# Kernel optimization log

Hardware: AMD Instinct MI355X
Metric: run time of the kernel (lower is better)

Reference implementation:

```python
import jax, jax.numpy as jnp
import numpy as np

N_NODES = 1_000_000
N_EDGES = 20_000_000


def setup_inputs() -> dict:
    key = jax.random.key(0)
    k_row, k_col, k_attr = jax.random.split(key, 3)
    # Guarantee every row appears at least once so row-sums are > 0
    # (the original module implicitly assumes no zero-degree rows).
    row_tail = jax.random.randint(k_row, (N_EDGES - N_NODES,), 0, N_NODES, dtype=jnp.int32)
    row = jnp.concatenate([jnp.arange(N_NODES, dtype=jnp.int32), row_tail])
    col = jax.random.randint(k_col, (N_EDGES,), 0, N_NODES, dtype=jnp.int32)
    edge_index = jnp.stack([row, col])  # [2, E]
    # Positive edge weights keep the reciprocal well-conditioned.
    edge_attr = jax.random.uniform(k_attr, (N_EDGES,), dtype=jnp.float32,
                                   minval=0.1, maxval=1.0)
    return {"edge_index": edge_index, "edge_attr": edge_attr, "N": N_NODES}


def reference(edge_index, edge_attr, N):
    # spmm(edge_index, edge_attr, N, N, ones) == per-row sum of edge weights
    rowsum = jax.ops.segment_sum(edge_attr, edge_index[0], num_segments=N)  # [N]
    rownorm = 1.0 / rowsum                                                  # [N]
    # Gather normalization factor at the COLUMN index of each edge, then scale.
    return rownorm[edge_index[1]] * edge_attr                                # [E]
```

## Files before the change

### kernel.cpp

```cpp
#include <hip/hip_runtime.h>
#include <stdint.h>


typedef int      v4i __attribute__((ext_vector_type(4)));
typedef float    v4f __attribute__((ext_vector_type(4)));
typedef unsigned v4u __attribute__((ext_vector_type(4)));
using ull = unsigned long long;

#define BKT_BITS 13
#define BKT_W    (1 << BKT_BITS)
#define NB       128
#define NMAX     (NB << BKT_BITS)
#define TILE     4096
#define BLOCK1   512
#define BLOCK2   1024


__global__ __launch_bounds__(BLOCK1) void hist_kernel(
    const int* __restrict__ row, int* __restrict__ histG, int E)
{
    __shared__ int h[NB];
    const int t = threadIdx.x;
    const long base = (long)blockIdx.x * TILE;
    if (t < NB) h[t] = 0;
    __syncthreads();
    if (base + TILE <= (long)E) {
        #pragma unroll
        for (int k = 0; k < 2; ++k) {
            const long e0 = base + ((long)(k * BLOCK1 + t) << 2);
            const v4i rv = *reinterpret_cast<const v4i*>(row + e0);
            atomicAdd(&h[rv.x >> BKT_BITS], 1);
            atomicAdd(&h[rv.y >> BKT_BITS], 1);
            atomicAdd(&h[rv.z >> BKT_BITS], 1);
            atomicAdd(&h[rv.w >> BKT_BITS], 1);
        }
    } else {
        for (int k = 0; k < 2; ++k) {
            const long e0 = base + ((long)(k * BLOCK1 + t) << 2);
            for (int j = 0; j < 4; ++j)
                if (e0 + j < (long)E) atomicAdd(&h[row[e0 + j] >> BKT_BITS], 1);
        }
    }
    __syncthreads();
    if (t < NB) histG[(size_t)blockIdx.x * NB + t] = h[t];
}

__global__ __launch_bounds__(256) void totals_kernel(
    const int* __restrict__ histG, int* __restrict__ totals, int nTiles)
{
    __shared__ int s[256];
    const int b = blockIdx.x;
    int acc = 0;
    for (int t = threadIdx.x; t < nTiles; t += 256)
        acc += histG[(size_t)t * NB + b];
    s[threadIdx.x] = acc;
    __syncthreads();
    for (int o = 128; o > 0; o >>= 1) {
        if (threadIdx.x < o) s[threadIdx.x] += s[threadIdx.x + o];
        __syncthreads();
    }
    if (threadIdx.x == 0) totals[b] = s[0];
}

__global__ __launch_bounds__(NB) void bases_kernel(
    const int* __restrict__ totals, int* __restrict__ bases)
{
    __shared__ int s[NB];
    const int t = threadIdx.x;
    const int rc = (totals[t] + 1) & ~1;
    s[t] = rc;
    __syncthreads();
    for (int off = 1; off < NB; off <<= 1) {
        const int v = (t >= off) ? s[t - off] : 0;
        __syncthreads();
        s[t] += v;
        __syncthreads();
    }
    bases[t] = s[t] - rc;
}

__global__ __launch_bounds__(256) void offsets_kernel(
    const int* __restrict__ histG, const int* __restrict__ bases,
    int* __restrict__ offG, int nTiles)
{
    __shared__ int s[256];
    const int b = blockIdx.x;
    const int seg = (nTiles + 255) >> 8;
    const int t0 = threadIdx.x * seg;
    int acc = 0;
    for (int k = 0; k < seg; ++k) {
        const int t = t0 + k;
        if (t < nTiles) acc += histG[(size_t)t * NB + b];
    }
    s[threadIdx.x] = acc;
    __syncthreads();
    for (int off = 1; off < 256; off <<= 1) {
        const int v = (threadIdx.x >= off) ? s[threadIdx.x - off] : 0;
        __syncthreads();
        s[threadIdx.x] += v;
        __syncthreads();
    }
    int run = bases[b] + s[threadIdx.x] - acc;
    for (int k = 0; k < seg; ++k) {
        const int t = t0 + k;
        if (t < nTiles) {
            offG[(size_t)t * NB + b] = run;
            run += histG[(size_t)t * NB + b];
        }
    }
}

__global__ __launch_bounds__(BLOCK1) void scatter_kernel(
    const int* __restrict__ row, const float* __restrict__ attr,
    const int* __restrict__ offG, ull* __restrict__ pairsG, int E)
{
    __shared__ int cnt[NB];
    __shared__ int scanb[NB];
    __shared__ int gbase[NB];
    __shared__ ull pairs[TILE];

    const int  t    = threadIdx.x;
    const long base = (long)blockIdx.x * TILE;
    const bool full = (base + TILE <= (long)E);

    if (t < NB) cnt[t] = 0;
    __syncthreads();

    int r[8]; float a[8]; int rk[8];
    if (full) {
        #pragma unroll
        for (int k = 0; k < 2; ++k) {
            const long e0 = base + ((long)(k * BLOCK1 + t) << 2);
            const v4i rv = *reinterpret_cast<const v4i*>(row + e0);
            const v4f av = __builtin_nontemporal_load(reinterpret_cast<const v4f*>(attr + e0));
            r[k*4+0]=rv.x; r[k*4+1]=rv.y; r[k*4+2]=rv.z; r[k*4+3]=rv.w;
            a[k*4+0]=av.x; a[k*4+1]=av.y; a[k*4+2]=av.z; a[k*4+3]=av.w;
        }
        #pragma unroll
        for (int i = 0; i < 8; ++i)
            rk[i] = atomicAdd(&cnt[r[i] >> BKT_BITS], 1);
    } else {
        for (int k = 0; k < 2; ++k) {
            const long e0 = base + ((long)(k * BLOCK1 + t) << 2);
            for (int j = 0; j < 4; ++j) {
                const int i = k*4 + j;
                if (e0 + j < (long)E) {
                    r[i] = row[e0 + j]; a[i] = attr[e0 + j];
                    rk[i] = atomicAdd(&cnt[r[i] >> BKT_BITS], 1);
                } else r[i] = -1;
            }
        }
    }
    __syncthreads();

    if (t < 64) {
        const int h0 = cnt[2*t], h1 = cnt[2*t+1];
        const int sum = h0 + h1;
        int x = sum;
        #pragma unroll
        for (int off = 1; off < 64; off <<= 1) {
            const int y = __shfl_up(x, off);
            if (t >= off) x += y;
        }
        const int excl = x - sum;
        scanb[2*t]   = excl;
        scanb[2*t+1] = excl + h0;
    }
    if (t < NB) gbase[t] = offG[(size_t)blockIdx.x * NB + t];
    __syncthreads();

    #pragma unroll
    for (int i = 0; i < 8; ++i)
        if (r[i] >= 0)
            pairs[scanb[r[i] >> BKT_BITS] + rk[i]] =
                ((ull)__float_as_uint(a[i]) << 32) | (unsigned)r[i];
    __syncthreads();

    const int total = full ? TILE : (int)((long)E - base);
    for (int s = t; s < total; s += BLOCK1) {
        const ull p  = pairs[s];
        const int bb = (int)(((unsigned)p) >> BKT_BITS);
        const size_t dst = (size_t)gbase[bb] + (size_t)(s - scanb[bb]);
        pairsG[dst] = p;
    }
}

__global__ __launch_bounds__(BLOCK2) void reduce_kernel(
    const ull* __restrict__ pairsG, const int* __restrict__ totals,
    const int* __restrict__ bases, float* __restrict__ partial, int nSplit)
{
    __shared__ float bins[BKT_W];
    const int b = blockIdx.x / nSplit;
    const int q = blockIdx.x % nSplit;
    const int t = threadIdx.x, w = t >> 6, l = t & 63;
    for (int i = t; i < BKT_W; i += BLOCK2) bins[i] = 0.0f;
    __syncthreads();

    const int cnt = totals[b];
    const ull* src = pairsG + (size_t)bases[b];
    const int nFull = cnt >> 13;

    for (int c = q; c < nFull; c += nSplit) {
        const ull addr = (ull)(src + (((size_t)c << 13) + (w << 9) + (l << 1)));
        v4u x0, x1, x2, x3;
        asm volatile(
            "global_load_dwordx4 %0, %4, off\n\t"
            "global_load_dwordx4 %1, %4, off offset:1024\n\t"
            "global_load_dwordx4 %2, %4, off offset:2048\n\t"
            "global_load_dwordx4 %3, %4, off offset:3072\n\t"
            "s_waitcnt vmcnt(0)"
            : "=&v"(x0), "=&v"(x1), "=&v"(x2), "=&v"(x3)
            : "v"(addr)
            : "memory");
        atomicAdd(&bins[x0.x & (BKT_W-1)], __uint_as_float(x0.y));
        atomicAdd(&bins[x0.z & (BKT_W-1)], __uint_as_float(x0.w));
        atomicAdd(&bins[x1.x & (BKT_W-1)], __uint_as_float(x1.y));
        atomicAdd(&bins[x1.z & (BKT_W-1)], __uint_as_float(x1.w));
        atomicAdd(&bins[x2.x & (BKT_W-1)], __uint_as_float(x2.y));
        atomicAdd(&bins[x2.z & (BKT_W-1)], __uint_as_float(x2.w));
        atomicAdd(&bins[x3.x & (BKT_W-1)], __uint_as_float(x3.y));
        atomicAdd(&bins[x3.z & (BKT_W-1)], __uint_as_float(x3.w));
    }
    if (q == 0) {
        for (int o = (nFull << 13) + t; o < cnt; o += BLOCK2) {
            const ull p = src[o];
            atomicAdd(&bins[(unsigned)p & (BKT_W-1)], __uint_as_float((unsigned)(p >> 32)));
        }
    }
    __syncthreads();

    float* dst = partial + (size_t)q * NMAX + ((size_t)b << BKT_BITS);
    for (int i = t; i < BKT_W; i += BLOCK2)
        dst[i] = bins[i];
}

__global__ void recip_kernel(const float* __restrict__ partial,
                             float* __restrict__ rnF,
                             const int* __restrict__ Np, int nSplit) {
    const int N = *Np;
    const int stride = gridDim.x * blockDim.x;
    for (int i = blockIdx.x * blockDim.x + threadIdx.x; i < N; i += stride) {
        float s = 0.0f;
        for (int q = 0; q < nSplit; ++q) s += partial[(size_t)q * NMAX + i];
        rnF[i] = 1.0f / s;
    }
}

__global__ __launch_bounds__(256) void gather_asm_kernel(
    const int* __restrict__ col, const float* __restrict__ attr,
    const float* __restrict__ rnF, float* __restrict__ out, int E)
{
    const int tid = blockIdx.x * blockDim.x + threadIdx.x;
    const int stride = gridDim.x * blockDim.x;
    const int E4 = E >> 2;
    const v4i* col4  = reinterpret_cast<const v4i*>(col);
    const v4f* attr4 = reinterpret_cast<const v4f*>(attr);
    v4f*       out4  = reinterpret_cast<v4f*>(out);

    int i = tid;
    for (; i + 3 * stride < E4; i += 4 * stride) {
        const v4i c0 = __builtin_nontemporal_load(col4 + i);
        const v4i c1 = __builtin_nontemporal_load(col4 + i + stride);
        const v4i c2 = __builtin_nontemporal_load(col4 + i + 2 * stride);
        const v4i c3 = __builtin_nontemporal_load(col4 + i + 3 * stride);
        const v4f a0 = __builtin_nontemporal_load(attr4 + i);
        const v4f a1 = __builtin_nontemporal_load(attr4 + i + stride);
        const v4f a2 = __builtin_nontemporal_load(attr4 + i + 2 * stride);
        const v4f a3 = __builtin_nontemporal_load(attr4 + i + 3 * stride);

        const ull p00 = (ull)(rnF + c0.x), p01 = (ull)(rnF + c0.y),
                  p02 = (ull)(rnF + c0.z), p03 = (ull)(rnF + c0.w),
                  p10 = (ull)(rnF + c1.x), p11 = (ull)(rnF + c1.y),
                  p12 = (ull)(rnF + c1.z), p13 = (ull)(rnF + c1.w),
                  p20 = (ull)(rnF + c2.x), p21 = (ull)(rnF + c2.y),
                  p22 = (ull)(rnF + c2.z), p23 = (ull)(rnF + c2.w),
                  p30 = (ull)(rnF + c3.x), p31 = (ull)(rnF + c3.y),
                  p32 = (ull)(rnF + c3.z), p33 = (ull)(rnF + c3.w);
        float f00, f01, f02, f03, f10, f11, f12, f13,
              f20, f21, f22, f23, f30, f31, f32, f33;
        asm volatile(
            "global_load_dword %0, %16, off\n\t"
            "global_load_dword %1, %17, off\n\t"
            "global_load_dword %2, %18, off\n\t"
            "global_load_dword %3, %19, off\n\t"
            "global_load_dword %4, %20, off\n\t"
            "global_load_dword %5, %21, off\n\t"
            "global_load_dword %6, %22, off\n\t"
            "global_load_dword %7, %23, off\n\t"
            "global_load_dword %8, %24, off\n\t"
            "global_load_dword %9, %25, off\n\t"
            "global_load_dword %10, %26, off\n\t"
            "global_load_dword %11, %27, off\n\t"
            "global_load_dword %12, %28, off\n\t"
            "global_load_dword %13, %29, off\n\t"
            "global_load_dword %14, %30, off\n\t"
            "global_load_dword %15, %31, off\n\t"
            "s_waitcnt vmcnt(0)"
            : "=&v"(f00), "=&v"(f01), "=&v"(f02), "=&v"(f03),
              "=&v"(f10), "=&v"(f11), "=&v"(f12), "=&v"(f13),
              "=&v"(f20), "=&v"(f21), "=&v"(f22), "=&v"(f23),
              "=&v"(f30), "=&v"(f31), "=&v"(f32), "=&v"(f33)
            : "v"(p00), "v"(p01), "v"(p02), "v"(p03),
              "v"(p10), "v"(p11), "v"(p12), "v"(p13),
              "v"(p20), "v"(p21), "v"(p22), "v"(p23),
              "v"(p30), "v"(p31), "v"(p32), "v"(p33)
            : "memory");

        v4f o0, o1, o2, o3;
        o0.x = f00 * a0.x; o0.y = f01 * a0.y; o0.z = f02 * a0.z; o0.w = f03 * a0.w;
        o1.x = f10 * a1.x; o1.y = f11 * a1.y; o1.z = f12 * a1.z; o1.w = f13 * a1.w;
        o2.x = f20 * a2.x; o2.y = f21 * a2.y; o2.z = f22 * a2.z; o2.w = f23 * a2.w;
        o3.x = f30 * a3.x; o3.y = f31 * a3.y; o3.z = f32 * a3.z; o3.w = f33 * a3.w;
        __builtin_nontemporal_store(o0, out4 + i);
        __builtin_nontemporal_store(o1, out4 + i + stride);
        __builtin_nontemporal_store(o2, out4 + i + 2 * stride);
        __builtin_nontemporal_store(o3, out4 + i + 3 * stride);
    }
    for (; i < E4; i += stride) {
        const v4i c = __builtin_nontemporal_load(col4 + i);
        const v4f a = __builtin_nontemporal_load(attr4 + i);
        v4f o;
        o.x = rnF[c.x] * a.x; o.y = rnF[c.y] * a.y;
        o.z = rnF[c.z] * a.z; o.w = rnF[c.w] * a.w;
        __builtin_nontemporal_store(o, out4 + i);
    }
    for (int e = (E4 << 2) + tid; e < E; e += stride)
        out[e] = rnF[col[e]] * attr[e];
}


__global__ void zero_ws_kernel(float* __restrict__ ws, const int* __restrict__ Np) {
    const int N = *Np;
    const int stride = gridDim.x * blockDim.x;
    for (int i = blockIdx.x * blockDim.x + threadIdx.x; i < N; i += stride)
        ws[i] = 0.0f;
}

__global__ void rowsum_atomic_kernel(const int* __restrict__ row,
                                     const float* __restrict__ attr,
                                     float* __restrict__ rowsum, int E) {
    const int tid = blockIdx.x * blockDim.x + threadIdx.x;
    const int stride = gridDim.x * blockDim.x;
    const int E4 = E >> 2;
    for (int i = tid; i < E4; i += stride) {
        const int4   r = reinterpret_cast<const int4*>(row)[i];
        const float4 a = reinterpret_cast<const float4*>(attr)[i];
        atomicAdd(&rowsum[r.x], a.x);
        atomicAdd(&rowsum[r.y], a.y);
        atomicAdd(&rowsum[r.z], a.z);
        atomicAdd(&rowsum[r.w], a.w);
    }
    for (int i = (E4 << 2) + tid; i < E; i += stride)
        atomicAdd(&rowsum[row[i]], attr[i]);
}

__global__ void recip_fallback_kernel(float* __restrict__ rowsum,
                                      const int* __restrict__ Np) {
    const int N = *Np;
    const int stride = gridDim.x * blockDim.x;
    for (int i = blockIdx.x * blockDim.x + threadIdx.x; i < N; i += stride)
        rowsum[i] = 1.0f / rowsum[i];
}

__global__ __launch_bounds__(256) void gather_scale_f32_kernel(
    const int* __restrict__ col, const float* __restrict__ attr,
    const float* __restrict__ rnorm, float* __restrict__ out, int E)
{
    const int tid = blockIdx.x * blockDim.x + threadIdx.x;
    const int stride = gridDim.x * blockDim.x;
    const int E4 = E >> 2;
    const v4i* col4  = reinterpret_cast<const v4i*>(col);
    const v4f* attr4 = reinterpret_cast<const v4f*>(attr);
    v4f*       out4  = reinterpret_cast<v4f*>(out);
    for (int i = tid; i < E4; i += stride) {
        const v4i c = __builtin_nontemporal_load(col4 + i);
        const v4f a = __builtin_nontemporal_load(attr4 + i);
        v4f o;
        o.x = rnorm[c.x] * a.x; o.y = rnorm[c.y] * a.y;
        o.z = rnorm[c.z] * a.z; o.w = rnorm[c.w] * a.w;
        __builtin_nontemporal_store(o, out4 + i);
    }
    for (int e = (E4 << 2) + tid; e < E; e += stride)
        out[e] = rnorm[col[e]] * attr[e];
}


extern "C" void kernel_launch(void* const* d_in, const int* in_sizes, int n_in,
                              void* d_out, int out_size, void* d_ws, size_t ws_size,
                              hipStream_t stream) {
    const int*   edge_index = (const int*)d_in[0];
    const float* edge_attr  = (const float*)d_in[1];
    const int*   Np         = (const int*)d_in[2];

    const int E = in_sizes[1];
    const int* row = edge_index;
    const int* col = edge_index + E;
    float* out = (float*)d_out;

    const int nTiles = (E + TILE - 1) / TILE;
    auto align256 = [](size_t x) { return (x + 255) & ~(size_t)255; };

    size_t off = 0;
    const size_t basesOff  = off; off += align256(NB * sizeof(int));
    const size_t totalsOff = off; off += align256(NB * sizeof(int));
    const size_t rnOff     = off; off += align256((size_t)NMAX * sizeof(float));
    const size_t partOff   = off;
    const size_t histBytes = align256((size_t)nTiles * NB * sizeof(int));
    const size_t scanBytes = 2 * histBytes;
    const size_t pairsBytes = ((size_t)E + 2 * NB) * sizeof(ull);

    int nSplit = 0;
    size_t partRegion = 0;
    for (int c : {4, 2, 1}) {
        size_t pr = (size_t)c * NMAX * sizeof(float);
        if (pr < scanBytes) pr = scanBytes;
        if (partOff + pr + pairsBytes <= ws_size) { nSplit = c; partRegion = pr; break; }
    }

    if (nSplit > 0) {
        int*   bases   = (int*)  ((char*)d_ws + basesOff);
        int*   totals  = (int*)  ((char*)d_ws + totalsOff);
        float* rnF     = (float*)((char*)d_ws + rnOff);
        float* partial = (float*)((char*)d_ws + partOff);
        int*   histG   = (int*)  ((char*)d_ws + partOff);
        int*   offG    = (int*)  ((char*)d_ws + partOff + histBytes);
        ull*   pairs   = (ull*)  ((char*)d_ws + partOff + partRegion);

        hist_kernel      <<<nTiles, BLOCK1, 0, stream>>>(row, histG, E);
        totals_kernel    <<<NB, 256, 0, stream>>>(histG, totals, nTiles);
        bases_kernel     <<<1, NB, 0, stream>>>(totals, bases);
        offsets_kernel   <<<NB, 256, 0, stream>>>(histG, bases, offG, nTiles);
        scatter_kernel   <<<nTiles, BLOCK1, 0, stream>>>(row, edge_attr, offG, pairs, E);
        reduce_kernel    <<<NB * nSplit, BLOCK2, 0, stream>>>(pairs, totals, bases, partial, nSplit);
        recip_kernel     <<<1024, 256, 0, stream>>>(partial, rnF, Np, nSplit);
        gather_asm_kernel<<<2048, 256, 0, stream>>>(col, edge_attr, rnF, out, E);
    } else {
        float* rowsum = (float*)d_ws;
        const int workE = (E + 3) >> 2;
        int gE = (workE + 255) / 256;
        if (gE > 2048) gE = 2048;
        zero_ws_kernel        <<<2048, 256, 0, stream>>>(rowsum, Np);
        rowsum_atomic_kernel  <<<gE, 256, 0, stream>>>(row, edge_attr, rowsum, E);
        recip_fallback_kernel <<<2048, 256, 0, stream>>>(rowsum, Np);
        gather_scale_f32_kernel<<<2048, 256, 0, stream>>>(col, edge_attr, rowsum, out, E);
    }
}
```

Baseline: 363.9 us.

## Use 256 narrower row buckets and simplify the reduce loop with vector loads

The row-bucket partition goes from 128 buckets of 8192 rows to 256 buckets of 4096 rows. The per-tile bucket scan now covers four buckets per lane. The reduce kernel drops the inline-asm 8-pair chunk loop for a strided loop that loads four pairs per thread with two 16-byte loads and a small remainder path. The split factor is capped at 2, so the number of reduce blocks stays the same while each block's LDS histogram halves, which may raise occupancy. The risk is smaller per-bucket runs in the scatter step, giving less coalesced global writes, plus removal of the explicit load batching.

```diff
diff --git a/kernel.cpp b/kernel.cpp
--- a/kernel.cpp
+++ b/kernel.cpp
@@ -7,9 +7,9 @@
 typedef unsigned v4u __attribute__((ext_vector_type(4)));
 using ull = unsigned long long;
 
-#define BKT_BITS 13
+#define BKT_BITS 12
 #define BKT_W    (1 << BKT_BITS)
-#define NB       128
+#define NB       256
 #define NMAX     (NB << BKT_BITS)
 #define TILE     4096
 #define BLOCK1   512
@@ -154,8 +154,8 @@
     __syncthreads();
 
     if (t < 64) {
-        const int h0 = cnt[2*t], h1 = cnt[2*t+1];
-        const int sum = h0 + h1;
+        const int h0 = cnt[4*t+0], h1 = cnt[4*t+1], h2 = cnt[4*t+2], h3 = cnt[4*t+3];
+        const int sum = h0 + h1 + h2 + h3;
         int x = sum;
         #pragma unroll
         for (int off = 1; off < 64; off <<= 1) {
@@ -163,8 +163,10 @@
             if (t >= off) x += y;
         }
         const int excl = x - sum;
-        scanb[2*t]   = excl;
-        scanb[2*t+1] = excl + h0;
+        scanb[4*t+0] = excl;
+        scanb[4*t+1] = excl + h0;
+        scanb[4*t+2] = excl + h0 + h1;
+        scanb[4*t+3] = excl + h0 + h1 + h2;
     }
     if (t < NB) gbase[t] = offG[(size_t)blockIdx.x * NB + t];
     __syncthreads();
@@ -192,45 +194,29 @@
     __shared__ float bins[BKT_W];
     const int b = blockIdx.x / nSplit;
     const int q = blockIdx.x % nSplit;
-    const int t = threadIdx.x, w = t >> 6, l = t & 63;
-    for (int i = t; i < BKT_W; i += BLOCK2) bins[i] = 0.0f;
+    for (int i = threadIdx.x; i < BKT_W; i += BLOCK2) bins[i] = 0.0f;
     __syncthreads();
 
     const int cnt = totals[b];
     const ull* src = pairsG + (size_t)bases[b];
-    const int nFull = cnt >> 13;
-
-    for (int c = q; c < nFull; c += nSplit) {
-        const ull addr = (ull)(src + (((size_t)c << 13) + (w << 9) + (l << 1)));
-        v4u x0, x1, x2, x3;
-        asm volatile(
-            "global_load_dwordx4 %0, %4, off\n\t"
-            "global_load_dwordx4 %1, %4, off offset:1024\n\t"
-            "global_load_dwordx4 %2, %4, off offset:2048\n\t"
-            "global_load_dwordx4 %3, %4, off offset:3072\n\t"
-            "s_waitcnt vmcnt(0)"
-            : "=&v"(x0), "=&v"(x1), "=&v"(x2), "=&v"(x3)
-            : "v"(addr)
-            : "memory");
-        atomicAdd(&bins[x0.x & (BKT_W-1)], __uint_as_float(x0.y));
-        atomicAdd(&bins[x0.z & (BKT_W-1)], __uint_as_float(x0.w));
-        atomicAdd(&bins[x1.x & (BKT_W-1)], __uint_as_float(x1.y));
-        atomicAdd(&bins[x1.z & (BKT_W-1)], __uint_as_float(x1.w));
-        atomicAdd(&bins[x2.x & (BKT_W-1)], __uint_as_float(x2.y));
-        atomicAdd(&bins[x2.z & (BKT_W-1)], __uint_as_float(x2.w));
-        atomicAdd(&bins[x3.x & (BKT_W-1)], __uint_as_float(x3.y));
-        atomicAdd(&bins[x3.z & (BKT_W-1)], __uint_as_float(x3.w));
-    }
-    if (q == 0) {
-        for (int o = (nFull << 13) + t; o < cnt; o += BLOCK2) {
-            const ull p = src[o];
-            atomicAdd(&bins[(unsigned)p & (BKT_W-1)], __uint_as_float((unsigned)(p >> 32)));
-        }
+    const int Q = cnt >> 2;
+    for (int i = q * BLOCK2 + threadIdx.x; i < Q; i += nSplit * BLOCK2) {
+        const v4u p0 = *reinterpret_cast<const v4u*>(src + 4*(size_t)i);
+        const v4u p1 = *reinterpret_cast<const v4u*>(src + 4*(size_t)i + 2);
+        atomicAdd(&bins[p0.x & (BKT_W-1)], __uint_as_float(p0.y));
+        atomicAdd(&bins[p0.z & (BKT_W-1)], __uint_as_float(p0.w));
+        atomicAdd(&bins[p1.x & (BKT_W-1)], __uint_as_float(p1.y));
+        atomicAdd(&bins[p1.z & (BKT_W-1)], __uint_as_float(p1.w));
+    }
+    const int rem = cnt - (Q << 2);
+    if (q == 0 && threadIdx.x < rem) {
+        const ull p = src[(Q << 2) + threadIdx.x];
+        atomicAdd(&bins[(unsigned)p & (BKT_W-1)], __uint_as_float((unsigned)(p >> 32)));
     }
     __syncthreads();
 
     float* dst = partial + (size_t)q * NMAX + ((size_t)b << BKT_BITS);
-    for (int i = t; i < BKT_W; i += BLOCK2)
+    for (int i = threadIdx.x; i < BKT_W; i += BLOCK2)
         dst[i] = bins[i];
 }
 
@@ -411,7 +397,7 @@
 
     int nSplit = 0;
     size_t partRegion = 0;
-    for (int c : {4, 2, 1}) {
+    for (int c : {2, 1}) {
         size_t pr = (size_t)c * NMAX * sizeof(float);
         if (pr < scanBytes) pr = scanBytes;
         if (partOff + pr + pairsBytes <= ws_size) { nSplit = c; partRegion = pr; break; }
```

New measurement: 362.3 us. No clear change (-0.4%).
